# Optimization experiments

Hardware: AMD Instinct MI355X
Metric: run time of the kernel (lower is better)

Reference implementation:

```python
import jax, jax.numpy as jnp
import numpy as np

NUM_BINS = 64  # num_bins_target == num_bins_source (defaults)
C_WIN = 1.0    # c_target == c_source (defaults)
EPS_LOG = 1e-12


def _normalise(x):
    # normalise_torch(x, 0.0, 1.0): global min-max rescale to [0, 1]
    x = x.astype(jnp.float32)
    return (x - x.min()) / (x.max() - x.min())


def _cubic_bspline(x):
    # Parzen cubic B-spline window (support |x| < 2)
    ax = jnp.abs(x)
    inner = (4.0 - 6.0 * ax * ax + 3.0 * ax * ax * ax) / 6.0
    outer = (2.0 - ax) ** 3 / 6.0
    return jnp.where(ax < 1.0, inner, jnp.where(ax < 2.0, outer, 0.0))


def setup_inputs() -> dict:
    key = jax.random.key(0)
    k1, k2 = jax.random.split(key)
    target = jax.random.uniform(k1, (2, 1, 96, 96, 96), dtype=jnp.float32)
    source = jax.random.uniform(k2, (2, 1, 96, 96, 96), dtype=jnp.float32)
    return {"target": target, "source": source}


def reference(target, source):
    # pre-processing: normalise to [0,1], flatten spatial dims -> (B, 1, N)
    t = _normalise(target).reshape(target.shape[0], target.shape[1], -1)
    s = _normalise(source).reshape(source.shape[0], source.shape[1], -1)

    # histogram bins (after normalisation max-min == 1)
    bw_t = (t.max() - t.min()) / NUM_BINS
    bw_s = (s.max() - s.min()) / NUM_BINS
    bins_t = jnp.arange(NUM_BINS, dtype=jnp.float32)[:, None] * bw_t  # (bins, 1)
    bins_s = jnp.arange(NUM_BINS, dtype=jnp.float32)[:, None] * bw_s
    eps_t = C_WIN * bw_t
    eps_s = C_WIN * bw_s

    # broadcast: (bins,1) - (B,1,N) -> (B, bins, N)
    W_t = _cubic_bspline((bins_t - t) / eps_t)
    W_s = _cubic_bspline((bins_s - s) / eps_s)

    # joint histogram: (B, bins_t, bins_s)
    hist_joint = jnp.einsum('bin,bjn->bij', W_t, W_s) / (eps_t * eps_s)

    # distributions (normalised over the WHOLE tensor, incl. batch, as in torch)
    p_joint = hist_joint / hist_joint.sum()
    p_t = p_joint.sum(axis=2)  # (B, bins_t)
    p_s = p_joint.sum(axis=1)  # (B, bins_s)

    # entropies per batch element
    H_t = -jnp.sum(p_t * jnp.log(p_t + EPS_LOG), axis=1)
    H_s = -jnp.sum(p_s * jnp.log(p_s + EPS_LOG), axis=1)
    H_j = -jnp.sum(p_joint * jnp.log(p_joint + EPS_LOG), axis=(1, 2))

    # NMI loss (nmi=True default)
    return -jnp.mean((H_t + H_s) / H_j)
```

## Files before the change

### kernel.cpp

```cpp
#include <hip/hip_runtime.h>
#include <math.h>

#define NBINS 64
#define BATCH_N 884736
#define NTOT   1769472
#define NCHUNK 13824
#define ROWB  80
#define TILE_B 5440
#define WAVE_B 10880
#define MROW 66
#define QS 190.0f
#define GBLK 864
#define GWAVES 1728
#define KBLK 512

#define OFF_GHIST 256
#define OFF_KBLK 36864
#define OFF_PART 65536

typedef int  v4i __attribute__((ext_vector_type(4)));

__device__ __forceinline__ unsigned fkey(float x){
    unsigned u = __float_as_uint(x);
    return (u & 0x80000000u) ? ~u : (u | 0x80000000u);
}
__device__ __forceinline__ float fdecode(unsigned k){
    return __uint_as_float((k & 0x80000000u) ? (k ^ 0x80000000u) : ~k);
}

__device__ __forceinline__ void bw4(float u, float w[4]){
    float um = 1.f - u;
    float u2 = u*u, um2 = um*um;
    w[0] = um2*um*(1.f/6.f);
    w[3] = u2*u*(1.f/6.f);
    w[1] = 0.6666666666666667f - u2 + 0.5f*u2*u;
    w[2] = 0.6666666666666667f - um2 + 0.5f*um2*um;
}

__global__ void __launch_bounds__(256)
k_minmax(const float4* __restrict__ t4, const float4* __restrict__ s4,
         int n4, uint4* __restrict__ kblk){
    __shared__ unsigned red[4][4];

    unsigned mt=0u, mnt=0u, ms=0u, mns=0u;
    int stride = gridDim.x * blockDim.x;
    for (int i = blockIdx.x*blockDim.x + threadIdx.x; i < n4; i += stride){
        float4 a = t4[i];
        float4 b = s4[i];
        mt  = max(mt,  max(max(fkey(a.x),  fkey(a.y)),  max(fkey(a.z),  fkey(a.w))));
        mnt = max(mnt, max(max(fkey(-a.x), fkey(-a.y)), max(fkey(-a.z), fkey(-a.w))));
        ms  = max(ms,  max(max(fkey(b.x),  fkey(b.y)),  max(fkey(b.z),  fkey(b.w))));
        mns = max(mns, max(max(fkey(-b.x), fkey(-b.y)), max(fkey(-b.z), fkey(-b.w))));
    }
    #pragma unroll
    for (int off = 32; off; off >>= 1){
        mt  = max(mt,  __shfl_down(mt,  off));
        mnt = max(mnt, __shfl_down(mnt, off));
        ms  = max(ms,  __shfl_down(ms,  off));
        mns = max(mns, __shfl_down(mns, off));
    }
    int wid = threadIdx.x >> 6;
    if ((threadIdx.x & 63) == 0){
        red[wid][0] = mt; red[wid][1] = mnt; red[wid][2] = ms; red[wid][3] = mns;
    }
    __syncthreads();
    if (threadIdx.x == 0){
        uint4 q;
        q.x = max(max(red[0][0], red[1][0]), max(red[2][0], red[3][0]));
        q.y = max(max(red[0][1], red[1][1]), max(red[2][1], red[3][1]));
        q.z = max(max(red[0][2], red[1][2]), max(red[2][2], red[3][2]));
        q.w = max(max(red[0][3], red[1][3]), max(red[2][3], red[3][3]));
        kblk[blockIdx.x] = q;
    }
}

__global__ void __launch_bounds__(128)
k_gemm(const float* __restrict__ t, const float* __restrict__ s,
       const uint4* __restrict__ kblk, float* __restrict__ ghist,
       float* __restrict__ part){
    __shared__ int4 smem4[1360];
    __shared__ unsigned kred[2][4];

    int lane = threadIdx.x & 63;
    int warp = threadIdx.x >> 6;
    int rrow = lane & 15;
    int kgrp = lane >> 4;
    int b = blockIdx.y;

    if (b == 0 && blockIdx.x < 8){
        #pragma unroll
        for (int k = 0; k < 8; ++k)
            ghist[blockIdx.x*1024 + k*128 + threadIdx.x] = 0.f;
    }

    {
        unsigned m0=0u, m1=0u, m2=0u, m3=0u;
        for (int i = threadIdx.x; i < KBLK; i += 128){
            uint4 q = kblk[i];
            m0 = max(m0, q.x); m1 = max(m1, q.y);
            m2 = max(m2, q.z); m3 = max(m3, q.w);
        }
        #pragma unroll
        for (int off = 32; off; off >>= 1){
            m0 = max(m0, __shfl_down(m0, off));
            m1 = max(m1, __shfl_down(m1, off));
            m2 = max(m2, __shfl_down(m2, off));
            m3 = max(m3, __shfl_down(m3, off));
        }
        if (lane == 0){
            kred[warp][0] = m0; kred[warp][1] = m1;
            kred[warp][2] = m2; kred[warp][3] = m3;
        }
        __syncthreads();
    }
    float tmax =  fdecode(max(kred[0][0], kred[1][0]));
    float tmin = -fdecode(max(kred[0][1], kred[1][1]));
    float smax =  fdecode(max(kred[0][2], kred[1][2]));
    float smin = -fdecode(max(kred[0][3], kred[1][3]));
    float tsc = 64.f / (tmax - tmin);
    float ssc = 64.f / (smax - smin);

    char* As = (char*)smem4 + warp*WAVE_B;
    char* Bs = As + TILE_B;

    {
        int4* wz = (int4*)As;
        int4 z4 = {0,0,0,0};
        #pragma unroll
        for (int i = 0; i < 11; ++i){
            int idx = i*64 + lane;
            if (idx < WAVE_B/16) wz[idx] = z4;
        }
    }

    const float* tb = t + (size_t)b*BATCH_N;
    const float* sb = s + (size_t)b*BATCH_N;

    v4i acc[4][4];
    #pragma unroll
    for (int i = 0; i < 4; ++i)
        #pragma unroll
        for (int j = 0; j < 4; ++j)
            acc[i][j] = (v4i){0,0,0,0};

    int c0 = blockIdx.x*2 + warp;
    float tq0 = tb[(size_t)c0*64 + lane];
    float sq0 = sb[(size_t)c0*64 + lane];
    float tq1 = tb[(size_t)(c0 + GWAVES)*64 + lane];
    float sq1 = sb[(size_t)(c0 + GWAVES)*64 + lane];

    #pragma unroll 2
    for (int it = 0; it < 8; ++it){
        int cpre = c0 + (it < 6 ? (it + 2)*GWAVES : 0);
        float tnn = tb[(size_t)cpre*64 + lane];
        float snn = sb[(size_t)cpre*64 + lane];

        float vt = (tq0 - tmin) * tsc;
        float vs = (sq0 - smin) * ssc;
        int it0 = (int)floorf(vt);
        int is0 = (int)floorf(vs);
        float wt[4], wsv[4];
        bw4(vt - (float)it0, wt);
        bw4(vs - (float)is0, wsv);

        char* pa = As + it0*ROWB + lane;
        char* pb = Bs + is0*ROWB + lane;
        #pragma unroll
        for (int k = 0; k < 4; ++k){
            pa[k*ROWB] = (char)__float2int_rn(wt[k]  * QS);
            pb[k*ROWB] = (char)__float2int_rn(wsv[k] * QS);
        }

        v4i af[4], bf[4];
        #pragma unroll
        for (int m = 0; m < 4; ++m)
            af[m] = *(const v4i*)(As + (m*16 + rrow + 1)*ROWB + kgrp*16);
        #pragma unroll
        for (int n = 0; n < 4; ++n)
            bf[n] = *(const v4i*)(Bs + (n*16 + rrow + 1)*ROWB + kgrp*16);
        #pragma unroll
        for (int m = 0; m < 4; ++m)
            #pragma unroll
            for (int n = 0; n < 4; ++n)
                acc[m][n] = __builtin_amdgcn_mfma_i32_16x16x64_i8(af[m], bf[n], acc[m][n], 0, 0, 0);

        __asm__ volatile("" ::: "memory");
        #pragma unroll
        for (int k = 0; k < 4; ++k){
            pa[k*ROWB] = 0;
            pb[k*ROWB] = 0;
        }

        tq0 = tq1; sq0 = sq1;
        tq1 = tnn; sq1 = snn;
    }

    const float dq = 1.f / (QS*QS);
    float* fm = (float*)smem4;
    __syncthreads();
    if (warp == 0){
        #pragma unroll
        for (int m = 0; m < 4; ++m)
            #pragma unroll
            for (int n = 0; n < 4; ++n)
                #pragma unroll
                for (int r = 0; r < 4; ++r)
                    fm[(m*16 + kgrp*4 + r)*MROW + n*16 + rrow] = (float)acc[m][n][r] * dq;
    }
    __syncthreads();
    if (warp == 1){
        #pragma unroll
        for (int m = 0; m < 4; ++m)
            #pragma unroll
            for (int n = 0; n < 4; ++n)
                #pragma unroll
                for (int r = 0; r < 4; ++r)
                    fm[(m*16 + kgrp*4 + r)*MROW + n*16 + rrow] += (float)acc[m][n][r] * dq;
    }
    __syncthreads();
    float* gp = part + ((size_t)(b*GBLK + blockIdx.x))*4096;
    for (int i = threadIdx.x; i < 4096; i += 128)
        gp[i] = fm[(i >> 6)*MROW + (i & 63)];
}

__global__ void __launch_bounds__(256)
k_reduce(const float* __restrict__ part, float* __restrict__ ghist){
    int b = blockIdx.y;
    int bin4 = (blockIdx.x*256 + threadIdx.x)*4;
    int p0 = blockIdx.z*32;
    const float* base = part + (size_t)(b*GBLK + p0)*4096 + bin4;
    float4 acc4 = {0.f,0.f,0.f,0.f};
    #pragma unroll
    for (int g = 0; g < 2; ++g){
        float4 v[16];
        #pragma unroll
        for (int i = 0; i < 16; ++i)
            v[i] = *(const float4*)(base + (size_t)(g*16 + i)*4096);
        float4 s;
        s.x = ((v[0].x+v[1].x)+(v[2].x+v[3].x)) + ((v[4].x+v[5].x)+(v[6].x+v[7].x))
            + ((v[8].x+v[9].x)+(v[10].x+v[11].x)) + ((v[12].x+v[13].x)+(v[14].x+v[15].x));
        s.y = ((v[0].y+v[1].y)+(v[2].y+v[3].y)) + ((v[4].y+v[5].y)+(v[6].y+v[7].y))
            + ((v[8].y+v[9].y)+(v[10].y+v[11].y)) + ((v[12].y+v[13].y)+(v[14].y+v[15].y));
        s.z = ((v[0].z+v[1].z)+(v[2].z+v[3].z)) + ((v[4].z+v[5].z)+(v[6].z+v[7].z))
            + ((v[8].z+v[9].z)+(v[10].z+v[11].z)) + ((v[12].z+v[13].z)+(v[14].z+v[15].z));
        s.w = ((v[0].w+v[1].w)+(v[2].w+v[3].w)) + ((v[4].w+v[5].w)+(v[6].w+v[7].w))
            + ((v[8].w+v[9].w)+(v[10].w+v[11].w)) + ((v[12].w+v[13].w)+(v[14].w+v[15].w));
        acc4.x += s.x; acc4.y += s.y; acc4.z += s.z; acc4.w += s.w;
    }
    float* g = ghist + b*4096 + bin4;
    unsafeAtomicAdd(&g[0], acc4.x);
    unsafeAtomicAdd(&g[1], acc4.y);
    unsafeAtomicAdd(&g[2], acc4.z);
    unsafeAtomicAdd(&g[3], acc4.w);
}

__device__ __forceinline__ float blockReduceSum(float v, float* red){
    #pragma unroll
    for (int off = 32; off; off >>= 1) v += __shfl_down(v, off);
    int wid = threadIdx.x >> 6, lane = threadIdx.x & 63;
    __syncthreads();
    if (lane == 0) red[wid] = v;
    __syncthreads();
    return red[0] + red[1] + red[2] + red[3];
}

__global__ void k_final(const float* __restrict__ hist, float* __restrict__ out){
    __shared__ float sh[2*4096];
    __shared__ float red[4];
    int tid = threadIdx.x;
    for (int i = tid; i < 8192; i += 256) sh[i] = hist[i];
    __syncthreads();

    float loc = 0.f;
    for (int i = tid; i < 8192; i += 256) loc += sh[i];
    float total = blockReduceSum(loc, red);
    float inv = 1.f / total;

    float nmi[2];
    for (int b = 0; b < 2; ++b){
        const float* h = sh + b*4096;
        float lj = 0.f;
        for (int i = tid; i < 4096; i += 256){
            float p = h[i]*inv;
            lj += p*logf(p + 1e-12f);
        }
        float Hj = -blockReduceSum(lj, red);
        float lt = 0.f;
        if (tid < 64){
            float r = 0.f;
            for (int j = 0; j < 64; ++j) r += h[tid*64 + j];
            float p = r*inv;
            lt = p*logf(p + 1e-12f);
        }
        float Ht = -blockReduceSum(lt, red);
        float ls = 0.f;
        if (tid < 64){
            float c = 0.f;
            for (int j = 0; j < 64; ++j) c += h[j*64 + tid];
            float p = c*inv;
            ls = p*logf(p + 1e-12f);
        }
        float Hs = -blockReduceSum(ls, red);
        nmi[b] = (Ht + Hs) / Hj;
    }
    if (tid == 0) out[0] = -0.5f*(nmi[0] + nmi[1]);
}

extern "C" void kernel_launch(void* const* d_in, const int* in_sizes, int n_in,
                              void* d_out, int out_size, void* d_ws, size_t ws_size,
                              hipStream_t stream) {
    const float* t = (const float*)d_in[0];
    const float* s = (const float*)d_in[1];
    float* out = (float*)d_out;
    float* ghist = (float*)((char*)d_ws + OFF_GHIST);
    uint4* kblk  = (uint4*)((char*)d_ws + OFF_KBLK);
    float* part  = (float*)((char*)d_ws + OFF_PART);

    k_minmax<<<KBLK, 256, 0, stream>>>((const float4*)t, (const float4*)s, NTOT/4, kblk);
    k_gemm<<<dim3(GBLK, 2), 128, 0, stream>>>(t, s, kblk, ghist, part);
    k_reduce<<<dim3(4, 2, 27), 256, 0, stream>>>(part, ghist);
    k_final<<<1, 256, 0, stream>>>(ghist, out);
}
```

Baseline: 105.1 us.

## Replace int8 MFMA joint-histogram GEMM with LDS float atomic scatter

Drops the int8 MFMA formulation that built sparse per-voxel B-spline weight tiles in LDS and multiplied them. Each voxel now adds its 4x4 outer-product weights straight into a padded per-block LDS histogram with float atomics. Each 256-thread block handles 8 voxels per thread, giving half as many blocks, and the reduce kernel sums 16 partials instead of 32. This removes the wasted dense MFMA work on mostly-zero tiles and the int8 quantisation error, but adds heavy LDS atomic contention on the uniform data.

```diff
diff --git a/kernel.cpp b/kernel.cpp
--- a/kernel.cpp
+++ b/kernel.cpp
@@ -4,21 +4,14 @@
 #define NBINS 64
 #define BATCH_N 884736
 #define NTOT   1769472
-#define NCHUNK 13824
-#define ROWB  80
-#define TILE_B 5440
-#define WAVE_B 10880
-#define MROW 66
-#define QS 190.0f
-#define GBLK 864
-#define GWAVES 1728
+#define GBLK 432
 #define KBLK 512
+#define HROW 68
+#define HSZ  4624
 
 #define OFF_GHIST 256
 #define OFF_KBLK 36864
 #define OFF_PART 65536
-
-typedef int  v4i __attribute__((ext_vector_type(4)));
 
 __device__ __forceinline__ unsigned fkey(float x){
     unsigned u = __float_as_uint(x);
@@ -74,184 +67,108 @@
     }
 }
 
-__global__ void __launch_bounds__(128)
-k_gemm(const float* __restrict__ t, const float* __restrict__ s,
+__global__ void __launch_bounds__(256)
+k_hist(const float* __restrict__ t, const float* __restrict__ s,
        const uint4* __restrict__ kblk, float* __restrict__ ghist,
        float* __restrict__ part){
-    __shared__ int4 smem4[1360];
-    __shared__ unsigned kred[2][4];
-
-    int lane = threadIdx.x & 63;
-    int warp = threadIdx.x >> 6;
-    int rrow = lane & 15;
-    int kgrp = lane >> 4;
+    __shared__ float h[HSZ];
+    __shared__ unsigned kred[4][4];
+
+    int tid = threadIdx.x;
+    int lane = tid & 63, warp = tid >> 6;
     int b = blockIdx.y;
 
     if (b == 0 && blockIdx.x < 8){
         #pragma unroll
-        for (int k = 0; k < 8; ++k)
-            ghist[blockIdx.x*1024 + k*128 + threadIdx.x] = 0.f;
-    }
-
-    {
-        unsigned m0=0u, m1=0u, m2=0u, m3=0u;
-        for (int i = threadIdx.x; i < KBLK; i += 128){
-            uint4 q = kblk[i];
-            m0 = max(m0, q.x); m1 = max(m1, q.y);
-            m2 = max(m2, q.z); m3 = max(m3, q.w);
-        }
-        #pragma unroll
-        for (int off = 32; off; off >>= 1){
-            m0 = max(m0, __shfl_down(m0, off));
-            m1 = max(m1, __shfl_down(m1, off));
-            m2 = max(m2, __shfl_down(m2, off));
-            m3 = max(m3, __shfl_down(m3, off));
-        }
-        if (lane == 0){
-            kred[warp][0] = m0; kred[warp][1] = m1;
-            kred[warp][2] = m2; kred[warp][3] = m3;
-        }
-        __syncthreads();
-    }
-    float tmax =  fdecode(max(kred[0][0], kred[1][0]));
-    float tmin = -fdecode(max(kred[0][1], kred[1][1]));
-    float smax =  fdecode(max(kred[0][2], kred[1][2]));
-    float smin = -fdecode(max(kred[0][3], kred[1][3]));
+        for (int k = 0; k < 4; ++k)
+            ghist[blockIdx.x*1024 + k*256 + tid] = 0.f;
+    }
+
+    const float4* t4 = (const float4*)(t + (size_t)b*BATCH_N) + (size_t)blockIdx.x*512;
+    const float4* s4 = (const float4*)(s + (size_t)b*BATCH_N) + (size_t)blockIdx.x*512;
+    float4 ta = t4[tid], tb = t4[tid + 256];
+    float4 sa = s4[tid], sb = s4[tid + 256];
+
+    for (int i = tid; i < HSZ; i += 256) h[i] = 0.f;
+
+    unsigned m0=0u, m1=0u, m2=0u, m3=0u;
+    #pragma unroll
+    for (int i = 0; i < 2; ++i){
+        uint4 q = kblk[tid + i*256];
+        m0 = max(m0, q.x); m1 = max(m1, q.y);
+        m2 = max(m2, q.z); m3 = max(m3, q.w);
+    }
+    #pragma unroll
+    for (int off = 32; off; off >>= 1){
+        m0 = max(m0, __shfl_down(m0, off));
+        m1 = max(m1, __shfl_down(m1, off));
+        m2 = max(m2, __shfl_down(m2, off));
+        m3 = max(m3, __shfl_down(m3, off));
+    }
+    if (lane == 0){
+        kred[warp][0] = m0; kred[warp][1] = m1;
+        kred[warp][2] = m2; kred[warp][3] = m3;
+    }
+    __syncthreads();
+
+    float tmax =  fdecode(max(max(kred[0][0], kred[1][0]), max(kred[2][0], kred[3][0])));
+    float tmin = -fdecode(max(max(kred[0][1], kred[1][1]), max(kred[2][1], kred[3][1])));
+    float smax =  fdecode(max(max(kred[0][2], kred[1][2]), max(kred[2][2], kred[3][2])));
+    float smin = -fdecode(max(max(kred[0][3], kred[1][3]), max(kred[2][3], kred[3][3])));
     float tsc = 64.f / (tmax - tmin);
     float ssc = 64.f / (smax - smin);
 
-    char* As = (char*)smem4 + warp*WAVE_B;
-    char* Bs = As + TILE_B;
-
-    {
-        int4* wz = (int4*)As;
-        int4 z4 = {0,0,0,0};
-        #pragma unroll
-        for (int i = 0; i < 11; ++i){
-            int idx = i*64 + lane;
-            if (idx < WAVE_B/16) wz[idx] = z4;
-        }
-    }
-
-    const float* tb = t + (size_t)b*BATCH_N;
-    const float* sb = s + (size_t)b*BATCH_N;
-
-    v4i acc[4][4];
-    #pragma unroll
-    for (int i = 0; i < 4; ++i)
-        #pragma unroll
-        for (int j = 0; j < 4; ++j)
-            acc[i][j] = (v4i){0,0,0,0};
-
-    int c0 = blockIdx.x*2 + warp;
-    float tq0 = tb[(size_t)c0*64 + lane];
-    float sq0 = sb[(size_t)c0*64 + lane];
-    float tq1 = tb[(size_t)(c0 + GWAVES)*64 + lane];
-    float sq1 = sb[(size_t)(c0 + GWAVES)*64 + lane];
-
-    #pragma unroll 2
-    for (int it = 0; it < 8; ++it){
-        int cpre = c0 + (it < 6 ? (it + 2)*GWAVES : 0);
-        float tnn = tb[(size_t)cpre*64 + lane];
-        float snn = sb[(size_t)cpre*64 + lane];
-
-        float vt = (tq0 - tmin) * tsc;
-        float vs = (sq0 - smin) * ssc;
-        int it0 = (int)floorf(vt);
-        int is0 = (int)floorf(vs);
-        float wt[4], wsv[4];
-        bw4(vt - (float)it0, wt);
-        bw4(vs - (float)is0, wsv);
-
-        char* pa = As + it0*ROWB + lane;
-        char* pb = Bs + is0*ROWB + lane;
-        #pragma unroll
-        for (int k = 0; k < 4; ++k){
-            pa[k*ROWB] = (char)__float2int_rn(wt[k]  * QS);
-            pb[k*ROWB] = (char)__float2int_rn(wsv[k] * QS);
-        }
-
-        v4i af[4], bf[4];
-        #pragma unroll
-        for (int m = 0; m < 4; ++m)
-            af[m] = *(const v4i*)(As + (m*16 + rrow + 1)*ROWB + kgrp*16);
-        #pragma unroll
-        for (int n = 0; n < 4; ++n)
-            bf[n] = *(const v4i*)(Bs + (n*16 + rrow + 1)*ROWB + kgrp*16);
-        #pragma unroll
-        for (int m = 0; m < 4; ++m)
-            #pragma unroll
-            for (int n = 0; n < 4; ++n)
-                acc[m][n] = __builtin_amdgcn_mfma_i32_16x16x64_i8(af[m], bf[n], acc[m][n], 0, 0, 0);
-
-        __asm__ volatile("" ::: "memory");
-        #pragma unroll
-        for (int k = 0; k < 4; ++k){
-            pa[k*ROWB] = 0;
-            pb[k*ROWB] = 0;
-        }
-
-        tq0 = tq1; sq0 = sq1;
-        tq1 = tnn; sq1 = snn;
-    }
-
-    const float dq = 1.f / (QS*QS);
-    float* fm = (float*)smem4;
-    __syncthreads();
-    if (warp == 0){
-        #pragma unroll
-        for (int m = 0; m < 4; ++m)
-            #pragma unroll
-            for (int n = 0; n < 4; ++n)
-                #pragma unroll
-                for (int r = 0; r < 4; ++r)
-                    fm[(m*16 + kgrp*4 + r)*MROW + n*16 + rrow] = (float)acc[m][n][r] * dq;
-    }
-    __syncthreads();
-    if (warp == 1){
-        #pragma unroll
-        for (int m = 0; m < 4; ++m)
-            #pragma unroll
-            for (int n = 0; n < 4; ++n)
-                #pragma unroll
-                for (int r = 0; r < 4; ++r)
-                    fm[(m*16 + kgrp*4 + r)*MROW + n*16 + rrow] += (float)acc[m][n][r] * dq;
-    }
+    #define VOX(tv, sv) do { \
+        float vt = ((tv) - tmin) * tsc; \
+        float vs = ((sv) - smin) * ssc; \
+        int it0 = (int)vt; \
+        int is0 = (int)vs; \
+        float wt[4], wsv[4]; \
+        bw4(vt - (float)it0, wt); \
+        bw4(vs - (float)is0, wsv); \
+        int bse = it0*HROW + is0; \
+        _Pragma("unroll") \
+        for (int k = 0; k < 4; ++k){ \
+            _Pragma("unroll") \
+            for (int j = 0; j < 4; ++j) \
+                atomicAdd(&h[bse + k*HROW + j], wt[k]*wsv[j]); \
+        } \
+    } while(0)
+
+    VOX(ta.x, sa.x); VOX(ta.y, sa.y); VOX(ta.z, sa.z); VOX(ta.w, sa.w);
+    VOX(tb.x, sb.x); VOX(tb.y, sb.y); VOX(tb.z, sb.z); VOX(tb.w, sb.w);
+    #undef VOX
+
     __syncthreads();
     float* gp = part + ((size_t)(b*GBLK + blockIdx.x))*4096;
-    for (int i = threadIdx.x; i < 4096; i += 128)
-        gp[i] = fm[(i >> 6)*MROW + (i & 63)];
+    for (int i = tid; i < 4096; i += 256)
+        gp[i] = h[((i >> 6) + 1)*HROW + (i & 63) + 1];
 }
 
 __global__ void __launch_bounds__(256)
 k_reduce(const float* __restrict__ part, float* __restrict__ ghist){
     int b = blockIdx.y;
     int bin4 = (blockIdx.x*256 + threadIdx.x)*4;
-    int p0 = blockIdx.z*32;
+    int p0 = blockIdx.z*16;
     const float* base = part + (size_t)(b*GBLK + p0)*4096 + bin4;
-    float4 acc4 = {0.f,0.f,0.f,0.f};
-    #pragma unroll
-    for (int g = 0; g < 2; ++g){
-        float4 v[16];
-        #pragma unroll
-        for (int i = 0; i < 16; ++i)
-            v[i] = *(const float4*)(base + (size_t)(g*16 + i)*4096);
-        float4 s;
-        s.x = ((v[0].x+v[1].x)+(v[2].x+v[3].x)) + ((v[4].x+v[5].x)+(v[6].x+v[7].x))
-            + ((v[8].x+v[9].x)+(v[10].x+v[11].x)) + ((v[12].x+v[13].x)+(v[14].x+v[15].x));
-        s.y = ((v[0].y+v[1].y)+(v[2].y+v[3].y)) + ((v[4].y+v[5].y)+(v[6].y+v[7].y))
-            + ((v[8].y+v[9].y)+(v[10].y+v[11].y)) + ((v[12].y+v[13].y)+(v[14].y+v[15].y));
-        s.z = ((v[0].z+v[1].z)+(v[2].z+v[3].z)) + ((v[4].z+v[5].z)+(v[6].z+v[7].z))
-            + ((v[8].z+v[9].z)+(v[10].z+v[11].z)) + ((v[12].z+v[13].z)+(v[14].z+v[15].z));
-        s.w = ((v[0].w+v[1].w)+(v[2].w+v[3].w)) + ((v[4].w+v[5].w)+(v[6].w+v[7].w))
-            + ((v[8].w+v[9].w)+(v[10].w+v[11].w)) + ((v[12].w+v[13].w)+(v[14].w+v[15].w));
-        acc4.x += s.x; acc4.y += s.y; acc4.z += s.z; acc4.w += s.w;
-    }
+    float4 v[16];
+    #pragma unroll
+    for (int i = 0; i < 16; ++i)
+        v[i] = *(const float4*)(base + (size_t)i*4096);
+    float4 s;
+    s.x = ((v[0].x+v[1].x)+(v[2].x+v[3].x)) + ((v[4].x+v[5].x)+(v[6].x+v[7].x))
+        + ((v[8].x+v[9].x)+(v[10].x+v[11].x)) + ((v[12].x+v[13].x)+(v[14].x+v[15].x));
+    s.y = ((v[0].y+v[1].y)+(v[2].y+v[3].y)) + ((v[4].y+v[5].y)+(v[6].y+v[7].y))
+        + ((v[8].y+v[9].y)+(v[10].y+v[11].y)) + ((v[12].y+v[13].y)+(v[14].y+v[15].y));
+    s.z = ((v[0].z+v[1].z)+(v[2].z+v[3].z)) + ((v[4].z+v[5].z)+(v[6].z+v[7].z))
+        + ((v[8].z+v[9].z)+(v[10].z+v[11].z)) + ((v[12].z+v[13].z)+(v[14].z+v[15].z));
+    s.w = ((v[0].w+v[1].w)+(v[2].w+v[3].w)) + ((v[4].w+v[5].w)+(v[6].w+v[7].w))
+        + ((v[8].w+v[9].w)+(v[10].w+v[11].w)) + ((v[12].w+v[13].w)+(v[14].w+v[15].w));
     float* g = ghist + b*4096 + bin4;
-    unsafeAtomicAdd(&g[0], acc4.x);
-    unsafeAtomicAdd(&g[1], acc4.y);
-    unsafeAtomicAdd(&g[2], acc4.z);
-    unsafeAtomicAdd(&g[3], acc4.w);
+    unsafeAtomicAdd(&g[0], s.x);
+    unsafeAtomicAdd(&g[1], s.y);
+    unsafeAtomicAdd(&g[2], s.z);
+    unsafeAtomicAdd(&g[3], s.w);
 }
 
 __device__ __forceinline__ float blockReduceSum(float v, float* red){
@@ -317,7 +234,7 @@
     float* part  = (float*)((char*)d_ws + OFF_PART);
 
     k_minmax<<<KBLK, 256, 0, stream>>>((const float4*)t, (const float4*)s, NTOT/4, kblk);
-    k_gemm<<<dim3(GBLK, 2), 128, 0, stream>>>(t, s, kblk, ghist, part);
+    k_hist<<<dim3(GBLK, 2), 256, 0, stream>>>(t, s, kblk, ghist, part);
     k_reduce<<<dim3(4, 2, 27), 256, 0, stream>>>(part, ghist);
     k_final<<<1, 256, 0, stream>>>(ghist, out);
 }
```

Result: slower. 253.7 us (+141.4%).

## Fuse partial-histogram reduction into GEMM kernel via atomics and drop reduce pass

Applied to the files above, without the earlier changes.

Removes the separate k_reduce kernel and the global partial-histogram buffer. k_gemm blocks now have four waves, each handling 16 chunks, and they merge their accumulators in shared memory before atomically adding to the global histogram. Zeroing of the histogram moves into k_minmax. This cuts one launch and the round trip of the partial buffer through global memory, but it adds heavy atomic contention: 432 blocks each do 4096 atomics onto 8192 addresses, and there are fewer blocks to spread over the CUs.

```diff
diff --git a/kernel.cpp b/kernel.cpp
--- a/kernel.cpp
+++ b/kernel.cpp
@@ -4,19 +4,17 @@
 #define NBINS 64
 #define BATCH_N 884736
 #define NTOT   1769472
-#define NCHUNK 13824
 #define ROWB  80
 #define TILE_B 5440
 #define WAVE_B 10880
 #define MROW 66
 #define QS 190.0f
-#define GBLK 864
-#define GWAVES 1728
+#define GBLK 216
+#define GWAVES 864
 #define KBLK 512
 
 #define OFF_GHIST 256
 #define OFF_KBLK 36864
-#define OFF_PART 65536
 
 typedef int  v4i __attribute__((ext_vector_type(4)));
 
@@ -39,8 +37,14 @@
 
 __global__ void __launch_bounds__(256)
 k_minmax(const float4* __restrict__ t4, const float4* __restrict__ s4,
-         int n4, uint4* __restrict__ kblk){
+         int n4, uint4* __restrict__ kblk, float* __restrict__ ghist){
     __shared__ unsigned red[4][4];
+
+    if (blockIdx.x < 8)
+        ghist[blockIdx.x*1024 + threadIdx.x] = 0.f,
+        ghist[blockIdx.x*1024 + 256 + threadIdx.x] = 0.f,
+        ghist[blockIdx.x*1024 + 512 + threadIdx.x] = 0.f,
+        ghist[blockIdx.x*1024 + 768 + threadIdx.x] = 0.f;
 
     unsigned mt=0u, mnt=0u, ms=0u, mns=0u;
     int stride = gridDim.x * blockDim.x;
@@ -74,29 +78,37 @@
     }
 }
 
-__global__ void __launch_bounds__(128)
+__global__ void __launch_bounds__(256)
 k_gemm(const float* __restrict__ t, const float* __restrict__ s,
-       const uint4* __restrict__ kblk, float* __restrict__ ghist,
-       float* __restrict__ part){
-    __shared__ int4 smem4[1360];
-    __shared__ unsigned kred[2][4];
-
-    int lane = threadIdx.x & 63;
-    int warp = threadIdx.x >> 6;
+       const uint4* __restrict__ kblk, float* __restrict__ ghist){
+    __shared__ int4 smem4[2720];
+    __shared__ unsigned kred[4][4];
+
+    int tid = threadIdx.x;
+    int lane = tid & 63;
+    int warp = tid >> 6;
     int rrow = lane & 15;
     int kgrp = lane >> 4;
     int b = blockIdx.y;
 
-    if (b == 0 && blockIdx.x < 8){
-        #pragma unroll
-        for (int k = 0; k < 8; ++k)
-            ghist[blockIdx.x*1024 + k*128 + threadIdx.x] = 0.f;
+    char* As = (char*)smem4 + warp*WAVE_B;
+    char* Bs = As + TILE_B;
+
+    {
+        int4* wz = (int4*)As;
+        int4 z4 = {0,0,0,0};
+        #pragma unroll
+        for (int i = 0; i < 11; ++i){
+            int idx = i*64 + lane;
+            if (idx < WAVE_B/16) wz[idx] = z4;
+        }
     }
 
     {
         unsigned m0=0u, m1=0u, m2=0u, m3=0u;
-        for (int i = threadIdx.x; i < KBLK; i += 128){
-            uint4 q = kblk[i];
+        #pragma unroll
+        for (int i = 0; i < 2; ++i){
+            uint4 q = kblk[tid + i*256];
             m0 = max(m0, q.x); m1 = max(m1, q.y);
             m2 = max(m2, q.z); m3 = max(m3, q.w);
         }
@@ -113,25 +125,12 @@
         }
         __syncthreads();
     }
-    float tmax =  fdecode(max(kred[0][0], kred[1][0]));
-    float tmin = -fdecode(max(kred[0][1], kred[1][1]));
-    float smax =  fdecode(max(kred[0][2], kred[1][2]));
-    float smin = -fdecode(max(kred[0][3], kred[1][3]));
+    float tmax =  fdecode(max(max(kred[0][0], kred[1][0]), max(kred[2][0], kred[3][0])));
+    float tmin = -fdecode(max(max(kred[0][1], kred[1][1]), max(kred[2][1], kred[3][1])));
+    float smax =  fdecode(max(max(kred[0][2], kred[1][2]), max(kred[2][2], kred[3][2])));
+    float smin = -fdecode(max(max(kred[0][3], kred[1][3]), max(kred[2][3], kred[3][3])));
     float tsc = 64.f / (tmax - tmin);
     float ssc = 64.f / (smax - smin);
-
-    char* As = (char*)smem4 + warp*WAVE_B;
-    char* Bs = As + TILE_B;
-
-    {
-        int4* wz = (int4*)As;
-        int4 z4 = {0,0,0,0};
-        #pragma unroll
-        for (int i = 0; i < 11; ++i){
-            int idx = i*64 + lane;
-            if (idx < WAVE_B/16) wz[idx] = z4;
-        }
-    }
 
     const float* tb = t + (size_t)b*BATCH_N;
     const float* sb = s + (size_t)b*BATCH_N;
@@ -143,15 +142,15 @@
         for (int j = 0; j < 4; ++j)
             acc[i][j] = (v4i){0,0,0,0};
 
-    int c0 = blockIdx.x*2 + warp;
+    int c0 = blockIdx.x*4 + warp;
     float tq0 = tb[(size_t)c0*64 + lane];
     float sq0 = sb[(size_t)c0*64 + lane];
     float tq1 = tb[(size_t)(c0 + GWAVES)*64 + lane];
     float sq1 = sb[(size_t)(c0 + GWAVES)*64 + lane];
 
     #pragma unroll 2
-    for (int it = 0; it < 8; ++it){
-        int cpre = c0 + (it < 6 ? (it + 2)*GWAVES : 0);
+    for (int it = 0; it < 16; ++it){
+        int cpre = c0 + (it < 14 ? (it + 2)*GWAVES : 0);
         float tnn = tb[(size_t)cpre*64 + lane];
         float snn = sb[(size_t)cpre*64 + lane];
 
@@ -196,62 +195,39 @@
     }
 
     const float dq = 1.f / (QS*QS);
-    float* fm = (float*)smem4;
-    __syncthreads();
-    if (warp == 0){
+    float* fmw = (float*)((char*)smem4 + (warp >> 1)*(2*WAVE_B));
+    __syncthreads();
+    if ((warp & 1) == 0){
         #pragma unroll
         for (int m = 0; m < 4; ++m)
             #pragma unroll
             for (int n = 0; n < 4; ++n)
                 #pragma unroll
                 for (int r = 0; r < 4; ++r)
-                    fm[(m*16 + kgrp*4 + r)*MROW + n*16 + rrow] = (float)acc[m][n][r] * dq;
-    }
-    __syncthreads();
-    if (warp == 1){
+                    fmw[(m*16 + kgrp*4 + r)*MROW + n*16 + rrow] = (float)acc[m][n][r] * dq;
+    }
+    __syncthreads();
+    if ((warp & 1) == 1){
         #pragma unroll
         for (int m = 0; m < 4; ++m)
             #pragma unroll
             for (int n = 0; n < 4; ++n)
                 #pragma unroll
                 for (int r = 0; r < 4; ++r)
-                    fm[(m*16 + kgrp*4 + r)*MROW + n*16 + rrow] += (float)acc[m][n][r] * dq;
-    }
-    __syncthreads();
-    float* gp = part + ((size_t)(b*GBLK + blockIdx.x))*4096;
-    for (int i = threadIdx.x; i < 4096; i += 128)
-        gp[i] = fm[(i >> 6)*MROW + (i & 63)];
-}
-
-__global__ void __launch_bounds__(256)
-k_reduce(const float* __restrict__ part, float* __restrict__ ghist){
-    int b = blockIdx.y;
-    int bin4 = (blockIdx.x*256 + threadIdx.x)*4;
-    int p0 = blockIdx.z*32;
-    const float* base = part + (size_t)(b*GBLK + p0)*4096 + bin4;
-    float4 acc4 = {0.f,0.f,0.f,0.f};
-    #pragma unroll
-    for (int g = 0; g < 2; ++g){
-        float4 v[16];
-        #pragma unroll
-        for (int i = 0; i < 16; ++i)
-            v[i] = *(const float4*)(base + (size_t)(g*16 + i)*4096);
-        float4 s;
-        s.x = ((v[0].x+v[1].x)+(v[2].x+v[3].x)) + ((v[4].x+v[5].x)+(v[6].x+v[7].x))
-            + ((v[8].x+v[9].x)+(v[10].x+v[11].x)) + ((v[12].x+v[13].x)+(v[14].x+v[15].x));
-        s.y = ((v[0].y+v[1].y)+(v[2].y+v[3].y)) + ((v[4].y+v[5].y)+(v[6].y+v[7].y))
-            + ((v[8].y+v[9].y)+(v[10].y+v[11].y)) + ((v[12].y+v[13].y)+(v[14].y+v[15].y));
-        s.z = ((v[0].z+v[1].z)+(v[2].z+v[3].z)) + ((v[4].z+v[5].z)+(v[6].z+v[7].z))
-            + ((v[8].z+v[9].z)+(v[10].z+v[11].z)) + ((v[12].z+v[13].z)+(v[14].z+v[15].z));
-        s.w = ((v[0].w+v[1].w)+(v[2].w+v[3].w)) + ((v[4].w+v[5].w)+(v[6].w+v[7].w))
-            + ((v[8].w+v[9].w)+(v[10].w+v[11].w)) + ((v[12].w+v[13].w)+(v[14].w+v[15].w));
-        acc4.x += s.x; acc4.y += s.y; acc4.z += s.z; acc4.w += s.w;
-    }
-    float* g = ghist + b*4096 + bin4;
-    unsafeAtomicAdd(&g[0], acc4.x);
-    unsafeAtomicAdd(&g[1], acc4.y);
-    unsafeAtomicAdd(&g[2], acc4.z);
-    unsafeAtomicAdd(&g[3], acc4.w);
+                    fmw[(m*16 + kgrp*4 + r)*MROW + n*16 + rrow] += (float)acc[m][n][r] * dq;
+    }
+    __syncthreads();
+    {
+        const float* fm0 = (const float*)smem4;
+        const float* fm1 = (const float*)((char*)smem4 + 2*WAVE_B);
+        float* g = ghist + b*4096;
+        #pragma unroll
+        for (int i = 0; i < 16; ++i){
+            int idx = i*256 + tid;
+            int l = (idx >> 6)*MROW + (idx & 63);
+            unsafeAtomicAdd(&g[idx], fm0[l] + fm1[l]);
+        }
+    }
 }
 
 __device__ __forceinline__ float blockReduceSum(float v, float* red){
@@ -314,10 +290,8 @@
     float* out = (float*)d_out;
     float* ghist = (float*)((char*)d_ws + OFF_GHIST);
     uint4* kblk  = (uint4*)((char*)d_ws + OFF_KBLK);
-    float* part  = (float*)((char*)d_ws + OFF_PART);
-
-    k_minmax<<<KBLK, 256, 0, stream>>>((const float4*)t, (const float4*)s, NTOT/4, kblk);
-    k_gemm<<<dim3(GBLK, 2), 128, 0, stream>>>(t, s, kblk, ghist, part);
-    k_reduce<<<dim3(4, 2, 27), 256, 0, stream>>>(part, ghist);
+
+    k_minmax<<<KBLK, 256, 0, stream>>>((const float4*)t, (const float4*)s, NTOT/4, kblk, ghist);
+    k_gemm<<<dim3(GBLK, 2), 256, 0, stream>>>(t, s, kblk, ghist);
     k_final<<<1, 256, 0, stream>>>(ghist, out);
 }
```

New measurement: 97.62 us. 1.08x faster.
